# Kernel tuning notes

Measured on AMD Instinct MI355X. Metric: run time of the kernel, lower is better.

## Reference

```python
import jax, jax.numpy as jnp
import numpy as np

N_SRC0, N_DST0, N_DST1 = 100000, 50000, 25000
E0, E1, D = 1600000, 800000, 128


def setup_inputs() -> dict:
    key = jax.random.key(0)
    k = jax.random.split(key, 8)
    return {
        "x": jax.random.normal(k[0], (N_SRC0, D), dtype=jnp.float32),
        "src0": jax.random.randint(k[1], (E0,), 0, N_SRC0, dtype=jnp.int32),
        "dst0": jax.random.randint(k[2], (E0,), 0, N_DST0, dtype=jnp.int32),
        "ew0": jax.random.uniform(k[3], (E0,), dtype=jnp.float32),
        "src1": jax.random.randint(k[4], (E1,), 0, N_DST0, dtype=jnp.int32),
        "dst1": jax.random.randint(k[5], (E1,), 0, N_DST1, dtype=jnp.int32),
        "ew1": jax.random.uniform(k[6], (E1,), dtype=jnp.float32),
        "n_dst0": N_DST0,
        "n_dst1": N_DST1,
    }


def _propagate(h, src, dst, ew, n_dst):
    # u_mul_e: gather src feature per edge and scale by edge weight; sum-reduce to dst
    m = h[src] * ew[:, None]                      # [E, D]
    return jax.ops.segment_sum(m, dst, num_segments=n_dst)  # [n_dst, D]


def reference(x, src0, dst0, ew0, src1, dst1, ew1, n_dst0, n_dst1):
    # LightGCN forward over 2 sampled blocks, mlp_list=None
    h = _propagate(x, src0, dst0, ew0, n_dst0)    # [n_dst0, D]
    h = _propagate(h, src1, dst1, ew1, n_dst1)    # [n_dst1, D]
    return h
```

## Files before the change

### kernel.cpp

```cpp
#include <hip/hip_runtime.h>


#define DIMS 128
#define BK   64
#define BKSH 6
#define CAP  4096
#define CH   8192

__device__ __forceinline__ unsigned bf16_1(float a) {
  unsigned u = __float_as_uint(a);
  return (u + 0x7fffu + ((u >> 16) & 1u)) >> 16;
}
__device__ __forceinline__ unsigned pack_bf16(float a, float b) {
  return bf16_1(a) | (bf16_1(b) << 16);
}

__global__ __launch_bounds__(256) void hist_cvt(
    const int* __restrict__ dst0, const int* __restrict__ dst1,
    const float* __restrict__ xf, uint4* __restrict__ xbf4,
    int* __restrict__ wgcnt0, int* __restrict__ wgcnt1,
    int E0, int E1, int NB0, int NB1, int NW0, int NW1, long long n8) {
  int b = blockIdx.x;
  if (b < NW0 + NW1) {
    __shared__ int hist[1024];
    const int s1 = (b >= NW0);
    const int w  = s1 ? b - NW0 : b;
    const int E  = s1 ? E1 : E0;
    const int NB = s1 ? NB1 : NB0;
    const int* dst = s1 ? dst1 : dst0;
    int* wgcnt = s1 ? wgcnt1 : wgcnt0;
    for (int i = threadIdx.x; i < NB; i += 256) hist[i] = 0;
    __syncthreads();
    const int beg = w * CH, end = min(beg + CH, E);
    for (int e = beg + threadIdx.x; e < end; e += 256)
      atomicAdd(&hist[dst[e] >> BKSH], 1);
    __syncthreads();
    for (int i = threadIdx.x; i < NB; i += 256)
      wgcnt[w * NB + i] = hist[i];
  } else {
    long long t = (long long)(b - NW0 - NW1) * 256 + threadIdx.x;
    if (t < n8) {
      const float4* xf4 = (const float4*)xf;
      float4 v0 = xf4[t * 2], v1 = xf4[t * 2 + 1];
      xbf4[t] = make_uint4(pack_bf16(v0.x, v0.y), pack_bf16(v0.z, v0.w),
                           pack_bf16(v1.x, v1.y), pack_bf16(v1.z, v1.w));
    }
  }
}

__global__ __launch_bounds__(256) void scan_cols(
    int* __restrict__ wgcnt0, int* __restrict__ wgcnt1,
    int* __restrict__ gcur, int2* __restrict__ rg0, int2* __restrict__ rg1,
    int NB0, int NB1, int NW0, int NW1) {
  __shared__ int part[256];
  int b = blockIdx.x;
  const int s1 = (b >= NB0);
  const int i = s1 ? b - NB0 : b;
  int* wgcnt = s1 ? wgcnt1 : wgcnt0;
  int2* rg   = s1 ? rg1 : rg0;
  const int NB = s1 ? NB1 : NB0;
  const int NW = s1 ? NW1 : NW0;
  const int t = threadIdx.x;
  int v = (t < NW) ? wgcnt[t * NB + i] : 0;
  part[t] = v;
  __syncthreads();
  for (int off = 1; off < 256; off <<= 1) {
    int u = (t >= off) ? part[t - off] : 0;
    __syncthreads();
    part[t] += u;
    __syncthreads();
  }
  if (t < NW) wgcnt[t * NB + i] = part[t] - v;
  if (t == 255) {
    int tot = part[255];
    int base = atomicAdd(&gcur[s1], tot);
    rg[i] = make_int2(base, base + tot);
  }
}

__global__ __launch_bounds__(512) void partition_k(
    const int* __restrict__ src0, const int* __restrict__ dst0,
    const float* __restrict__ ew0, const int* __restrict__ src1,
    const int* __restrict__ dst1, const float* __restrict__ ew1,
    const int* __restrict__ wgcnt0, const int* __restrict__ wgcnt1,
    const int2* __restrict__ rg0, const int2* __restrict__ rg1,
    int2* __restrict__ payl0, int2* __restrict__ payl1,
    int E0, int E1, int NB0, int NB1, int NW0, int NW1) {
  __shared__ int cur[1024];
  int b = blockIdx.x;
  const int s1 = (b >= NW0);
  const int w  = s1 ? b - NW0 : b;
  const int E  = s1 ? E1 : E0;
  const int NB = s1 ? NB1 : NB0;
  const int* src = s1 ? src1 : src0;
  const int* dst = s1 ? dst1 : dst0;
  const float* ew = s1 ? ew1 : ew0;
  const int* wgcnt = s1 ? wgcnt1 : wgcnt0;
  const int2* rg = s1 ? rg1 : rg0;
  int2* payl = s1 ? payl1 : payl0;
  for (int i = threadIdx.x; i < NB; i += 512)
    cur[i] = rg[i].x + wgcnt[w * NB + i];
  __syncthreads();
  const int beg = w * CH, end = min(beg + CH, E);
  for (int e = beg + threadIdx.x; e < end; e += 512) {
    int d = dst[e];
    int pos = atomicAdd(&cur[d >> BKSH], 1);
    payl[pos] = make_int2(src[e],
                          (int)((bf16_1(ew[e]) << 16) | (unsigned)(d & (BK - 1))));
  }
}

#define EDGE_BLOCK(p, wgt, u)                                   \
  {                                                             \
    a0 += __uint_as_float((u).x << 16) * (wgt);                 \
    a1 += __uint_as_float((u).x & 0xffff0000u) * (wgt);         \
    a2 += __uint_as_float((u).y << 16) * (wgt);                 \
    a3 += __uint_as_float((u).y & 0xffff0000u) * (wgt);         \
    a4 += __uint_as_float((u).z << 16) * (wgt);                 \
    a5 += __uint_as_float((u).z & 0xffff0000u) * (wgt);         \
    a6 += __uint_as_float((u).w << 16) * (wgt);                 \
    a7 += __uint_as_float((u).w & 0xffff0000u) * (wgt);         \
  }

template <bool OUT_BF16>
__global__ __launch_bounds__(512) void gather_bkt(
    const uint4* __restrict__ feat, const int2* __restrict__ rg,
    const int2* __restrict__ payl, void* __restrict__ outp, int n_dst) {
  __shared__ int2 lp[CAP];
  __shared__ int cnt[BK], base[BK], cnt2[BK];
  const int b = blockIdx.x;
  const int tid = threadIdx.x;
  const int2 r = rg[b];
  const int n = r.y - r.x;
  const int nin = min(n, CAP);
  if (tid < BK) { cnt[tid] = 0; cnt2[tid] = 0; }
  __syncthreads();
  for (int j = tid; j < nin; j += 512)
    atomicAdd(&cnt[payl[r.x + j].y & (BK - 1)], 1);
  __syncthreads();
  if (tid < 64) {
    int v = cnt[tid];
    int s = v;
    for (int off = 1; off < 64; off <<= 1) {
      int u = __shfl_up(s, off);
      if (tid >= off) s += u;
    }
    base[tid] = s - v;
  }
  __syncthreads();
  for (int j = tid; j < nin; j += 512) {
    int2 p = payl[r.x + j];
    int dl = p.y & (BK - 1);
    int pos = base[dl] + atomicAdd(&cnt2[dl], 1);
    lp[pos] = p;
  }
  __syncthreads();
  const int wave = tid >> 6;
  const int lane = tid & 63;
  const int rr = lane >> 4;
  const int c  = lane & 15;
  for (int dl = wave; dl < BK; dl += 8) {
    const int row = b * BK + dl;
    if (row >= n_dst) break;
    const int bg = base[dl];
    const int en = bg + cnt[dl];
    float a0 = 0.f, a1 = 0.f, a2 = 0.f, a3 = 0.f;
    float a4 = 0.f, a5 = 0.f, a6 = 0.f, a7 = 0.f;
    for (int j = bg; j < en; j += 16) {
      const int jj0 = j + rr;
      const int jj1 = j + 4 + rr;
      const int jj2 = j + 8 + rr;
      const int jj3 = j + 12 + rr;
      int2 p0 = (jj0 < en) ? lp[jj0] : make_int2(0, 0);
      int2 p1 = (jj1 < en) ? lp[jj1] : make_int2(0, 0);
      int2 p2 = (jj2 < en) ? lp[jj2] : make_int2(0, 0);
      int2 p3 = (jj3 < en) ? lp[jj3] : make_int2(0, 0);
      uint4 u0 = feat[(size_t)p0.x * 16 + c];
      uint4 u1 = feat[(size_t)p1.x * 16 + c];
      uint4 u2 = feat[(size_t)p2.x * 16 + c];
      uint4 u3 = feat[(size_t)p3.x * 16 + c];
      float w0 = __uint_as_float((unsigned)p0.y & 0xffff0000u);
      float w1 = __uint_as_float((unsigned)p1.y & 0xffff0000u);
      float w2 = __uint_as_float((unsigned)p2.y & 0xffff0000u);
      float w3 = __uint_as_float((unsigned)p3.y & 0xffff0000u);
      EDGE_BLOCK(p0, w0, u0);
      EDGE_BLOCK(p1, w1, u1);
      EDGE_BLOCK(p2, w2, u2);
      EDGE_BLOCK(p3, w3, u3);
    }
    if (n > CAP) {
      for (int j = CAP; j < n; j += 4) {
        int jj = j + rr;
        int2 p = (jj < n) ? payl[r.x + jj] : make_int2(0, 0);
        bool mine = (jj < n) && ((p.y & (BK - 1)) == dl);
        float wgt = mine ? __uint_as_float((unsigned)p.y & 0xffff0000u) : 0.f;
        uint4 u = feat[(size_t)p.x * 16 + c];
        EDGE_BLOCK(p, wgt, u);
      }
    }
    a0 += __shfl_xor(a0, 16); a0 += __shfl_xor(a0, 32);
    a1 += __shfl_xor(a1, 16); a1 += __shfl_xor(a1, 32);
    a2 += __shfl_xor(a2, 16); a2 += __shfl_xor(a2, 32);
    a3 += __shfl_xor(a3, 16); a3 += __shfl_xor(a3, 32);
    a4 += __shfl_xor(a4, 16); a4 += __shfl_xor(a4, 32);
    a5 += __shfl_xor(a5, 16); a5 += __shfl_xor(a5, 32);
    a6 += __shfl_xor(a6, 16); a6 += __shfl_xor(a6, 32);
    a7 += __shfl_xor(a7, 16); a7 += __shfl_xor(a7, 32);
    if (OUT_BF16) {
      if (rr == 0) {
        ((uint4*)outp)[(size_t)row * 16 + c] =
            make_uint4(pack_bf16(a0, a1), pack_bf16(a2, a3),
                       pack_bf16(a4, a5), pack_bf16(a6, a7));
      }
    } else {
      if (rr < 2) {
        ((float4*)outp)[(size_t)row * 32 + c * 2 + rr] =
            (rr == 0) ? make_float4(a0, a1, a2, a3)
                      : make_float4(a4, a5, a6, a7);
      }
    }
  }
}

#define COLG 32
__global__ __launch_bounds__(256) void prop_atomic(
    const float* __restrict__ x, const int* __restrict__ src,
    const int* __restrict__ dst, const float* __restrict__ ew,
    float* __restrict__ out, int E) {
  long long idx = (long long)blockIdx.x * blockDim.x + threadIdx.x;
  long long total = (long long)E * COLG;
  if (idx >= total) return;
  int e = (int)(idx >> 5);
  int cg = (int)(idx & 31);
  int s = src[e];
  int d = dst[e];
  float w = ew[e];
  const float4 v = *reinterpret_cast<const float4*>(x + (size_t)s * DIMS + cg * 4);
  float* o = out + (size_t)d * DIMS + cg * 4;
  atomicAdd(o + 0, v.x * w);
  atomicAdd(o + 1, v.y * w);
  atomicAdd(o + 2, v.z * w);
  atomicAdd(o + 3, v.w * w);
}


static inline size_t align_up(size_t v, size_t a) { return (v + a - 1) / a * a; }

extern "C" void kernel_launch(void* const* d_in, const int* in_sizes, int n_in,
                              void* d_out, int out_size, void* d_ws, size_t ws_size,
                              hipStream_t stream) {
  const float* x    = (const float*)d_in[0];
  const int*   src0 = (const int*)d_in[1];
  const int*   dst0 = (const int*)d_in[2];
  const float* ew0  = (const float*)d_in[3];
  const int*   src1 = (const int*)d_in[4];
  const int*   dst1 = (const int*)d_in[5];
  const float* ew1  = (const float*)d_in[6];

  const int N_SRC0 = in_sizes[0] / DIMS;
  const int E0 = in_sizes[1];
  const int E1 = in_sizes[4];
  const int N_DST0 = 50000;
  const int N_DST1 = 25000;

  const int NB0 = (N_DST0 + BK - 1) / BK;
  const int NB1 = (N_DST1 + BK - 1) / BK;
  const int NW0 = (E0 + CH - 1) / CH;
  const int NW1 = (E1 + CH - 1) / CH;

  float* out = (float*)d_out;

  char* ws = (char*)d_ws;
  size_t off = 0;
  uint4* xb    = (uint4*)(ws + off); off = align_up(off + (size_t)N_SRC0 * 64 * 4, 16);
  uint4* hb    = (uint4*)(ws + off); off = align_up(off + (size_t)N_DST0 * 64 * 4, 16);
  int* wgcnt0  = (int*)(ws + off);   off = align_up(off + (size_t)NW0 * NB0 * 4, 16);
  int* wgcnt1  = (int*)(ws + off);   off = align_up(off + (size_t)NW1 * NB1 * 4, 16);
  int* gcur    = (int*)(ws + off);   off = align_up(off + 2 * 4, 16);
  int2* rg0    = (int2*)(ws + off);  off = align_up(off + (size_t)NB0 * 8, 16);
  int2* rg1    = (int2*)(ws + off);  off = align_up(off + (size_t)NB1 * 8, 16);
  int2* payl0  = (int2*)(ws + off);  off = align_up(off + (size_t)E0 * 8, 16);
  int2* payl1  = (int2*)(ws + off);  off = align_up(off + (size_t)E1 * 8, 16);
  const size_t needed = off;

  if (ws_size < needed) {
    float* h = (float*)d_ws;
    hipMemsetAsync(h, 0, (size_t)N_DST0 * DIMS * 4, stream);
    hipMemsetAsync(out, 0, (size_t)N_DST1 * DIMS * 4, stream);
    long long t0 = (long long)E0 * COLG;
    prop_atomic<<<(int)((t0 + 255) / 256), 256, 0, stream>>>(x, src0, dst0, ew0, h, E0);
    long long t1 = (long long)E1 * COLG;
    prop_atomic<<<(int)((t1 + 255) / 256), 256, 0, stream>>>(h, src1, dst1, ew1, out, E1);
    return;
  }

  const long long n8 = (long long)N_SRC0 * 16;
  const int cvtBlocks = (int)((n8 + 255) / 256);

  hipMemsetAsync(gcur, 0, 2 * 4, stream);

  hist_cvt<<<NW0 + NW1 + cvtBlocks, 256, 0, stream>>>(
      dst0, dst1, x, xb, wgcnt0, wgcnt1, E0, E1, NB0, NB1, NW0, NW1, n8);

  scan_cols<<<NB0 + NB1, 256, 0, stream>>>(wgcnt0, wgcnt1, gcur, rg0, rg1,
                                           NB0, NB1, NW0, NW1);

  partition_k<<<NW0 + NW1, 512, 0, stream>>>(
      src0, dst0, ew0, src1, dst1, ew1, wgcnt0, wgcnt1, rg0, rg1,
      payl0, payl1, E0, E1, NB0, NB1, NW0, NW1);

  gather_bkt<true><<<NB0, 512, 0, stream>>>(xb, rg0, payl0, (void*)hb, N_DST0);

  gather_bkt<false><<<NB1, 512, 0, stream>>>(hb, rg1, payl1, (void*)out, N_DST1);
}
```

Baseline: 168.9 us.

## Quantize gathered node features to int8 with per-row scales

Replaces the bf16 copies of the input features and the intermediate layer with int8 values plus a per-row float scale. The row scale is folded into the edge weight when payloads are staged in shared memory. This halves the bytes fetched per gathered row in both random-access gather passes, at the cost of much lower precision, which may break accuracy tolerances. It also swizzles the chunk-to-block mapping in the histogram and partition kernels, and the main gather loop loses its 4-way unroll.

Result: no change. 169.3 us (+0.2%).

```diff
diff --git a/kernel.cpp b/kernel.cpp
--- a/kernel.cpp
+++ b/kernel.cpp
@@ -11,20 +11,23 @@
   unsigned u = __float_as_uint(a);
   return (u + 0x7fffu + ((u >> 16) & 1u)) >> 16;
 }
-__device__ __forceinline__ unsigned pack_bf16(float a, float b) {
-  return bf16_1(a) | (bf16_1(b) << 16);
+
+__device__ __forceinline__ int chunk_swz(int b, int NW) {
+  const int q = NW >> 3, r = NW & 7, x = b & 7;
+  return (x < r ? x * (q + 1) : r * (q + 1) + (x - r) * q) + (b >> 3);
 }
 
 __global__ __launch_bounds__(256) void hist_cvt(
     const int* __restrict__ dst0, const int* __restrict__ dst1,
-    const float* __restrict__ xf, uint4* __restrict__ xbf4,
+    const float* __restrict__ xf, uint2* __restrict__ xq,
+    float* __restrict__ xscale,
     int* __restrict__ wgcnt0, int* __restrict__ wgcnt1,
-    int E0, int E1, int NB0, int NB1, int NW0, int NW1, long long n8) {
+    int E0, int E1, int NB0, int NB1, int NW0, int NW1, int NSRC) {
   int b = blockIdx.x;
   if (b < NW0 + NW1) {
     __shared__ int hist[1024];
     const int s1 = (b >= NW0);
-    const int w  = s1 ? b - NW0 : b;
+    const int w  = s1 ? chunk_swz(b - NW0, NW1) : chunk_swz(b, NW0);
     const int E  = s1 ? E1 : E0;
     const int NB = s1 ? NB1 : NB0;
     const int* dst = s1 ? dst1 : dst0;
@@ -38,12 +41,31 @@
     for (int i = threadIdx.x; i < NB; i += 256)
       wgcnt[w * NB + i] = hist[i];
   } else {
-    long long t = (long long)(b - NW0 - NW1) * 256 + threadIdx.x;
-    if (t < n8) {
+    int gi = (b - NW0 - NW1) * 256 + threadIdx.x;
+    int row = gi >> 4, c = gi & 15;
+    if (row < NSRC) {
       const float4* xf4 = (const float4*)xf;
-      float4 v0 = xf4[t * 2], v1 = xf4[t * 2 + 1];
-      xbf4[t] = make_uint4(pack_bf16(v0.x, v0.y), pack_bf16(v0.z, v0.w),
-                           pack_bf16(v1.x, v1.y), pack_bf16(v1.z, v1.w));
+      float4 v0 = xf4[(size_t)row * 32 + c * 2];
+      float4 v1 = xf4[(size_t)row * 32 + c * 2 + 1];
+      float m = fmaxf(fmaxf(fmaxf(fabsf(v0.x), fabsf(v0.y)),
+                            fmaxf(fabsf(v0.z), fabsf(v0.w))),
+                      fmaxf(fmaxf(fabsf(v1.x), fabsf(v1.y)),
+                            fmaxf(fabsf(v1.z), fabsf(v1.w))));
+      m = fmaxf(m, __shfl_xor(m, 1));
+      m = fmaxf(m, __shfl_xor(m, 2));
+      m = fmaxf(m, __shfl_xor(m, 4));
+      m = fmaxf(m, __shfl_xor(m, 8));
+      float inv = (m > 0.f) ? 127.0f / m : 0.f;
+      int q0 = (int)rintf(v0.x * inv), q1 = (int)rintf(v0.y * inv);
+      int q2 = (int)rintf(v0.z * inv), q3 = (int)rintf(v0.w * inv);
+      int q4 = (int)rintf(v1.x * inv), q5 = (int)rintf(v1.y * inv);
+      int q6 = (int)rintf(v1.z * inv), q7 = (int)rintf(v1.w * inv);
+      unsigned lo = (q0 & 255) | ((q1 & 255) << 8) |
+                    ((q2 & 255) << 16) | ((q3 & 255) << 24);
+      unsigned hi = (q4 & 255) | ((q5 & 255) << 8) |
+                    ((q6 & 255) << 16) | ((q7 & 255) << 24);
+      xq[(size_t)row * 16 + c] = make_uint2(lo, hi);
+      if (c == 0) xscale[row] = m * (1.0f / 127.0f);
     }
   }
 }
@@ -89,7 +111,7 @@
   __shared__ int cur[1024];
   int b = blockIdx.x;
   const int s1 = (b >= NW0);
-  const int w  = s1 ? b - NW0 : b;
+  const int w  = s1 ? chunk_swz(b - NW0, NW1) : chunk_swz(b, NW0);
   const int E  = s1 ? E1 : E0;
   const int NB = s1 ? NB1 : NB0;
   const int* src = s1 ? src1 : src0;
@@ -110,22 +132,23 @@
   }
 }
 
-#define EDGE_BLOCK(p, wgt, u)                                   \
+#define EDGE_BLOCK8(ws, u)                                      \
   {                                                             \
-    a0 += __uint_as_float((u).x << 16) * (wgt);                 \
-    a1 += __uint_as_float((u).x & 0xffff0000u) * (wgt);         \
-    a2 += __uint_as_float((u).y << 16) * (wgt);                 \
-    a3 += __uint_as_float((u).y & 0xffff0000u) * (wgt);         \
-    a4 += __uint_as_float((u).z << 16) * (wgt);                 \
-    a5 += __uint_as_float((u).z & 0xffff0000u) * (wgt);         \
-    a6 += __uint_as_float((u).w << 16) * (wgt);                 \
-    a7 += __uint_as_float((u).w & 0xffff0000u) * (wgt);         \
-  }
-
-template <bool OUT_BF16>
+    a0 += (float)((int)((u).x << 24) >> 24) * (ws);             \
+    a1 += (float)((int)((u).x << 16) >> 24) * (ws);             \
+    a2 += (float)((int)((u).x << 8) >> 24) * (ws);              \
+    a3 += (float)((int)(u).x >> 24) * (ws);                     \
+    a4 += (float)((int)((u).y << 24) >> 24) * (ws);             \
+    a5 += (float)((int)((u).y << 16) >> 24) * (ws);             \
+    a6 += (float)((int)((u).y << 8) >> 24) * (ws);              \
+    a7 += (float)((int)(u).y >> 24) * (ws);                     \
+  }
+
+template <bool OUT_I8>
 __global__ __launch_bounds__(512) void gather_bkt(
-    const uint4* __restrict__ feat, const int2* __restrict__ rg,
-    const int2* __restrict__ payl, void* __restrict__ outp, int n_dst) {
+    const uint2* __restrict__ feat, const float* __restrict__ scl,
+    const int2* __restrict__ rg, const int2* __restrict__ payl,
+    void* __restrict__ outp, float* __restrict__ oscale, int n_dst) {
   __shared__ int2 lp[CAP];
   __shared__ int cnt[BK], base[BK], cnt2[BK];
   const int b = blockIdx.x;
@@ -151,8 +174,9 @@
   for (int j = tid; j < nin; j += 512) {
     int2 p = payl[r.x + j];
     int dl = p.y & (BK - 1);
+    float ws = __uint_as_float((unsigned)p.y & 0xffff0000u) * scl[p.x];
     int pos = base[dl] + atomicAdd(&cnt2[dl], 1);
-    lp[pos] = p;
+    lp[pos] = make_int2(p.x, (int)((bf16_1(ws) << 16) | (unsigned)dl));
   }
   __syncthreads();
   const int wave = tid >> 6;
@@ -166,36 +190,22 @@
     const int en = bg + cnt[dl];
     float a0 = 0.f, a1 = 0.f, a2 = 0.f, a3 = 0.f;
     float a4 = 0.f, a5 = 0.f, a6 = 0.f, a7 = 0.f;
-    for (int j = bg; j < en; j += 16) {
-      const int jj0 = j + rr;
-      const int jj1 = j + 4 + rr;
-      const int jj2 = j + 8 + rr;
-      const int jj3 = j + 12 + rr;
-      int2 p0 = (jj0 < en) ? lp[jj0] : make_int2(0, 0);
-      int2 p1 = (jj1 < en) ? lp[jj1] : make_int2(0, 0);
-      int2 p2 = (jj2 < en) ? lp[jj2] : make_int2(0, 0);
-      int2 p3 = (jj3 < en) ? lp[jj3] : make_int2(0, 0);
-      uint4 u0 = feat[(size_t)p0.x * 16 + c];
-      uint4 u1 = feat[(size_t)p1.x * 16 + c];
-      uint4 u2 = feat[(size_t)p2.x * 16 + c];
-      uint4 u3 = feat[(size_t)p3.x * 16 + c];
-      float w0 = __uint_as_float((unsigned)p0.y & 0xffff0000u);
-      float w1 = __uint_as_float((unsigned)p1.y & 0xffff0000u);
-      float w2 = __uint_as_float((unsigned)p2.y & 0xffff0000u);
-      float w3 = __uint_as_float((unsigned)p3.y & 0xffff0000u);
-      EDGE_BLOCK(p0, w0, u0);
-      EDGE_BLOCK(p1, w1, u1);
-      EDGE_BLOCK(p2, w2, u2);
-      EDGE_BLOCK(p3, w3, u3);
+    for (int j = bg; j < en; j += 4) {
+      int jj = j + rr;
+      int2 p = (jj < en) ? lp[jj] : make_int2(0, 0);
+      float ws = __uint_as_float((unsigned)p.y & 0xffff0000u);
+      uint2 u = feat[(size_t)p.x * 16 + c];
+      EDGE_BLOCK8(ws, u);
     }
     if (n > CAP) {
       for (int j = CAP; j < n; j += 4) {
         int jj = j + rr;
         int2 p = (jj < n) ? payl[r.x + jj] : make_int2(0, 0);
         bool mine = (jj < n) && ((p.y & (BK - 1)) == dl);
-        float wgt = mine ? __uint_as_float((unsigned)p.y & 0xffff0000u) : 0.f;
-        uint4 u = feat[(size_t)p.x * 16 + c];
-        EDGE_BLOCK(p, wgt, u);
+        float ws = mine
+            ? __uint_as_float((unsigned)p.y & 0xffff0000u) * scl[p.x] : 0.f;
+        uint2 u = feat[(size_t)p.x * 16 + c];
+        EDGE_BLOCK8(ws, u);
       }
     }
     a0 += __shfl_xor(a0, 16); a0 += __shfl_xor(a0, 32);
@@ -206,12 +216,30 @@
     a5 += __shfl_xor(a5, 16); a5 += __shfl_xor(a5, 32);
     a6 += __shfl_xor(a6, 16); a6 += __shfl_xor(a6, 32);
     a7 += __shfl_xor(a7, 16); a7 += __shfl_xor(a7, 32);
-    if (OUT_BF16) {
+    if (OUT_I8) {
+      float m = fmaxf(fmaxf(fmaxf(fabsf(a0), fabsf(a1)),
+                            fmaxf(fabsf(a2), fabsf(a3))),
+                      fmaxf(fmaxf(fabsf(a4), fabsf(a5)),
+                            fmaxf(fabsf(a6), fabsf(a7))));
+      m = fmaxf(m, __shfl_xor(m, 1));
+      m = fmaxf(m, __shfl_xor(m, 2));
+      m = fmaxf(m, __shfl_xor(m, 4));
+      m = fmaxf(m, __shfl_xor(m, 8));
+      m = fmaxf(m, __shfl_xor(m, 16));
+      m = fmaxf(m, __shfl_xor(m, 32));
+      float inv = (m > 0.f) ? 127.0f / m : 0.f;
       if (rr == 0) {
-        ((uint4*)outp)[(size_t)row * 16 + c] =
-            make_uint4(pack_bf16(a0, a1), pack_bf16(a2, a3),
-                       pack_bf16(a4, a5), pack_bf16(a6, a7));
+        int q0 = (int)rintf(a0 * inv), q1 = (int)rintf(a1 * inv);
+        int q2 = (int)rintf(a2 * inv), q3 = (int)rintf(a3 * inv);
+        int q4 = (int)rintf(a4 * inv), q5 = (int)rintf(a5 * inv);
+        int q6 = (int)rintf(a6 * inv), q7 = (int)rintf(a7 * inv);
+        unsigned lo = (q0 & 255) | ((q1 & 255) << 8) |
+                      ((q2 & 255) << 16) | ((q3 & 255) << 24);
+        unsigned hi = (q4 & 255) | ((q5 & 255) << 8) |
+                      ((q6 & 255) << 16) | ((q7 & 255) << 24);
+        ((uint2*)outp)[(size_t)row * 16 + c] = make_uint2(lo, hi);
       }
+      if (lane == 0) oscale[row] = m * (1.0f / 127.0f);
     } else {
       if (rr < 2) {
         ((float4*)outp)[(size_t)row * 32 + c * 2 + rr] =
@@ -272,15 +300,17 @@
 
   char* ws = (char*)d_ws;
   size_t off = 0;
-  uint4* xb    = (uint4*)(ws + off); off = align_up(off + (size_t)N_SRC0 * 64 * 4, 16);
-  uint4* hb    = (uint4*)(ws + off); off = align_up(off + (size_t)N_DST0 * 64 * 4, 16);
-  int* wgcnt0  = (int*)(ws + off);   off = align_up(off + (size_t)NW0 * NB0 * 4, 16);
-  int* wgcnt1  = (int*)(ws + off);   off = align_up(off + (size_t)NW1 * NB1 * 4, 16);
-  int* gcur    = (int*)(ws + off);   off = align_up(off + 2 * 4, 16);
-  int2* rg0    = (int2*)(ws + off);  off = align_up(off + (size_t)NB0 * 8, 16);
-  int2* rg1    = (int2*)(ws + off);  off = align_up(off + (size_t)NB1 * 8, 16);
-  int2* payl0  = (int2*)(ws + off);  off = align_up(off + (size_t)E0 * 8, 16);
-  int2* payl1  = (int2*)(ws + off);  off = align_up(off + (size_t)E1 * 8, 16);
+  uint2* xq     = (uint2*)(ws + off); off = align_up(off + (size_t)N_SRC0 * 16 * 8, 16);
+  float* xscale = (float*)(ws + off); off = align_up(off + (size_t)N_SRC0 * 4, 16);
+  uint2* hq     = (uint2*)(ws + off); off = align_up(off + (size_t)N_DST0 * 16 * 8, 16);
+  float* hscale = (float*)(ws + off); off = align_up(off + (size_t)N_DST0 * 4, 16);
+  int* wgcnt0   = (int*)(ws + off);   off = align_up(off + (size_t)NW0 * NB0 * 4, 16);
+  int* wgcnt1   = (int*)(ws + off);   off = align_up(off + (size_t)NW1 * NB1 * 4, 16);
+  int* gcur     = (int*)(ws + off);   off = align_up(off + 2 * 4, 16);
+  int2* rg0     = (int2*)(ws + off);  off = align_up(off + (size_t)NB0 * 8, 16);
+  int2* rg1     = (int2*)(ws + off);  off = align_up(off + (size_t)NB1 * 8, 16);
+  int2* payl0   = (int2*)(ws + off);  off = align_up(off + (size_t)E0 * 8, 16);
+  int2* payl1   = (int2*)(ws + off);  off = align_up(off + (size_t)E1 * 8, 16);
   const size_t needed = off;
 
   if (ws_size < needed) {
@@ -294,13 +324,13 @@
     return;
   }
 
-  const long long n8 = (long long)N_SRC0 * 16;
-  const int cvtBlocks = (int)((n8 + 255) / 256);
+  const int cvtBlocks = (N_SRC0 * 16 + 255) / 256;
 
   hipMemsetAsync(gcur, 0, 2 * 4, stream);
 
   hist_cvt<<<NW0 + NW1 + cvtBlocks, 256, 0, stream>>>(
-      dst0, dst1, x, xb, wgcnt0, wgcnt1, E0, E1, NB0, NB1, NW0, NW1, n8);
+      dst0, dst1, x, xq, xscale, wgcnt0, wgcnt1,
+      E0, E1, NB0, NB1, NW0, NW1, N_SRC0);
 
   scan_cols<<<NB0 + NB1, 256, 0, stream>>>(wgcnt0, wgcnt1, gcur, rg0, rg1,
                                            NB0, NB1, NW0, NW1);
@@ -309,7 +339,9 @@
       src0, dst0, ew0, src1, dst1, ew1, wgcnt0, wgcnt1, rg0, rg1,
       payl0, payl1, E0, E1, NB0, NB1, NW0, NW1);
 
-  gather_bkt<true><<<NB0, 512, 0, stream>>>(xb, rg0, payl0, (void*)hb, N_DST0);
-
-  gather_bkt<false><<<NB1, 512, 0, stream>>>(hb, rg1, payl1, (void*)out, N_DST1);
-}
+  gather_bkt<true><<<NB0, 512, 0, stream>>>(
+      xq, xscale, rg0, payl0, (void*)hq, hscale, N_DST0);
+
+  gather_bkt<false><<<NB1, 512, 0, stream>>>(
+      hq, hscale, rg1, payl1, (void*)out, (float*)nullptr, N_DST1);
+}
```

## Process two destination rows per wave in gather and swizzle chunk order

Applied to the files above, without the earlier changes.

Each wave in the bucketed gather kernel now accumulates two destination rows at once (dl and dl+8), interleaving their edge loads. This gives two independent gather streams per iteration instead of a four-way unroll over one row's edge list, which cuts tail waste for short rows and balances per-row degree. It also permutes which edge chunk each workgroup handles in the histogram and partition kernels so that consecutive blocks touch spread-out chunks. The cost is more accumulator registers and more lanes idle when the two rows differ in degree.

Measured after the change: 168.5 us. About the same (-0.3%).

```diff
diff --git a/kernel.cpp b/kernel.cpp
--- a/kernel.cpp
+++ b/kernel.cpp
@@ -13,6 +13,11 @@
 }
 __device__ __forceinline__ unsigned pack_bf16(float a, float b) {
   return bf16_1(a) | (bf16_1(b) << 16);
+}
+
+__device__ __forceinline__ int chunk_swz(int b, int NW) {
+  const int q = NW >> 3, r = NW & 7, x = b & 7;
+  return (x < r ? x * (q + 1) : r * (q + 1) + (x - r) * q) + (b >> 3);
 }
 
 __global__ __launch_bounds__(256) void hist_cvt(
@@ -24,7 +29,7 @@
   if (b < NW0 + NW1) {
     __shared__ int hist[1024];
     const int s1 = (b >= NW0);
-    const int w  = s1 ? b - NW0 : b;
+    const int w  = s1 ? chunk_swz(b - NW0, NW1) : chunk_swz(b, NW0);
     const int E  = s1 ? E1 : E0;
     const int NB = s1 ? NB1 : NB0;
     const int* dst = s1 ? dst1 : dst0;
@@ -89,7 +94,7 @@
   __shared__ int cur[1024];
   int b = blockIdx.x;
   const int s1 = (b >= NW0);
-  const int w  = s1 ? b - NW0 : b;
+  const int w  = s1 ? chunk_swz(b - NW0, NW1) : chunk_swz(b, NW0);
   const int E  = s1 ? E1 : E0;
   const int NB = s1 ? NB1 : NB0;
   const int* src = s1 ? src1 : src0;
@@ -110,7 +115,7 @@
   }
 }
 
-#define EDGE_BLOCK(p, wgt, u)                                   \
+#define ACC8(a0,a1,a2,a3,a4,a5,a6,a7, wgt, u)                   \
   {                                                             \
     a0 += __uint_as_float((u).x << 16) * (wgt);                 \
     a1 += __uint_as_float((u).x & 0xffff0000u) * (wgt);         \
@@ -159,43 +164,41 @@
   const int lane = tid & 63;
   const int rr = lane >> 4;
   const int c  = lane & 15;
-  for (int dl = wave; dl < BK; dl += 8) {
-    const int row = b * BK + dl;
-    if (row >= n_dst) break;
-    const int bg = base[dl];
-    const int en = bg + cnt[dl];
+  for (int dl = wave; dl < BK; dl += 16) {
+    const int rowA = b * BK + dl;
+    const int rowB = b * BK + dl + 8;
+    if (rowA >= n_dst) break;
+    const bool hasB = (rowB < n_dst);
+    const int bgA = base[dl];
+    const int lA = cnt[dl];
+    const int bgB = hasB ? base[dl + 8] : 0;
+    const int lB = hasB ? cnt[dl + 8] : 0;
+    const int lmax = max(lA, lB);
     float a0 = 0.f, a1 = 0.f, a2 = 0.f, a3 = 0.f;
     float a4 = 0.f, a5 = 0.f, a6 = 0.f, a7 = 0.f;
-    for (int j = bg; j < en; j += 16) {
-      const int jj0 = j + rr;
-      const int jj1 = j + 4 + rr;
-      const int jj2 = j + 8 + rr;
-      const int jj3 = j + 12 + rr;
-      int2 p0 = (jj0 < en) ? lp[jj0] : make_int2(0, 0);
-      int2 p1 = (jj1 < en) ? lp[jj1] : make_int2(0, 0);
-      int2 p2 = (jj2 < en) ? lp[jj2] : make_int2(0, 0);
-      int2 p3 = (jj3 < en) ? lp[jj3] : make_int2(0, 0);
-      uint4 u0 = feat[(size_t)p0.x * 16 + c];
-      uint4 u1 = feat[(size_t)p1.x * 16 + c];
-      uint4 u2 = feat[(size_t)p2.x * 16 + c];
-      uint4 u3 = feat[(size_t)p3.x * 16 + c];
-      float w0 = __uint_as_float((unsigned)p0.y & 0xffff0000u);
-      float w1 = __uint_as_float((unsigned)p1.y & 0xffff0000u);
-      float w2 = __uint_as_float((unsigned)p2.y & 0xffff0000u);
-      float w3 = __uint_as_float((unsigned)p3.y & 0xffff0000u);
-      EDGE_BLOCK(p0, w0, u0);
-      EDGE_BLOCK(p1, w1, u1);
-      EDGE_BLOCK(p2, w2, u2);
-      EDGE_BLOCK(p3, w3, u3);
+    float b0 = 0.f, b1 = 0.f, b2 = 0.f, b3 = 0.f;
+    float b4 = 0.f, b5 = 0.f, b6 = 0.f, b7 = 0.f;
+    for (int k = rr; k < lmax; k += 4) {
+      int2 pA = (k < lA) ? lp[bgA + k] : make_int2(0, 0);
+      int2 pB = (k < lB) ? lp[bgB + k] : make_int2(0, 0);
+      uint4 uA = feat[(size_t)pA.x * 16 + c];
+      uint4 uB = feat[(size_t)pB.x * 16 + c];
+      float wA = __uint_as_float((unsigned)pA.y & 0xffff0000u);
+      float wB = __uint_as_float((unsigned)pB.y & 0xffff0000u);
+      ACC8(a0, a1, a2, a3, a4, a5, a6, a7, wA, uA);
+      ACC8(b0, b1, b2, b3, b4, b5, b6, b7, wB, uB);
     }
     if (n > CAP) {
-      for (int j = CAP; j < n; j += 4) {
-        int jj = j + rr;
-        int2 p = (jj < n) ? payl[r.x + jj] : make_int2(0, 0);
-        bool mine = (jj < n) && ((p.y & (BK - 1)) == dl);
-        float wgt = mine ? __uint_as_float((unsigned)p.y & 0xffff0000u) : 0.f;
+      for (int j = CAP + rr; j < n; j += 4) {
+        int2 p = payl[r.x + j];
+        int pdl = p.y & (BK - 1);
+        float wA = (pdl == dl)
+            ? __uint_as_float((unsigned)p.y & 0xffff0000u) : 0.f;
+        float wB = (hasB && pdl == dl + 8)
+            ? __uint_as_float((unsigned)p.y & 0xffff0000u) : 0.f;
         uint4 u = feat[(size_t)p.x * 16 + c];
-        EDGE_BLOCK(p, wgt, u);
+        ACC8(a0, a1, a2, a3, a4, a5, a6, a7, wA, u);
+        ACC8(b0, b1, b2, b3, b4, b5, b6, b7, wB, u);
       }
     }
     a0 += __shfl_xor(a0, 16); a0 += __shfl_xor(a0, 32);
@@ -206,17 +209,33 @@
     a5 += __shfl_xor(a5, 16); a5 += __shfl_xor(a5, 32);
     a6 += __shfl_xor(a6, 16); a6 += __shfl_xor(a6, 32);
     a7 += __shfl_xor(a7, 16); a7 += __shfl_xor(a7, 32);
+    b0 += __shfl_xor(b0, 16); b0 += __shfl_xor(b0, 32);
+    b1 += __shfl_xor(b1, 16); b1 += __shfl_xor(b1, 32);
+    b2 += __shfl_xor(b2, 16); b2 += __shfl_xor(b2, 32);
+    b3 += __shfl_xor(b3, 16); b3 += __shfl_xor(b3, 32);
+    b4 += __shfl_xor(b4, 16); b4 += __shfl_xor(b4, 32);
+    b5 += __shfl_xor(b5, 16); b5 += __shfl_xor(b5, 32);
+    b6 += __shfl_xor(b6, 16); b6 += __shfl_xor(b6, 32);
+    b7 += __shfl_xor(b7, 16); b7 += __shfl_xor(b7, 32);
     if (OUT_BF16) {
       if (rr == 0) {
-        ((uint4*)outp)[(size_t)row * 16 + c] =
+        ((uint4*)outp)[(size_t)rowA * 16 + c] =
             make_uint4(pack_bf16(a0, a1), pack_bf16(a2, a3),
                        pack_bf16(a4, a5), pack_bf16(a6, a7));
+        if (hasB)
+          ((uint4*)outp)[(size_t)rowB * 16 + c] =
+              make_uint4(pack_bf16(b0, b1), pack_bf16(b2, b3),
+                         pack_bf16(b4, b5), pack_bf16(b6, b7));
       }
     } else {
       if (rr < 2) {
-        ((float4*)outp)[(size_t)row * 32 + c * 2 + rr] =
+        ((float4*)outp)[(size_t)rowA * 32 + c * 2 + rr] =
             (rr == 0) ? make_float4(a0, a1, a2, a3)
                       : make_float4(a4, a5, a6, a7);
+        if (hasB)
+          ((float4*)outp)[(size_t)rowB * 32 + c * 2 + rr] =
+              (rr == 0) ? make_float4(b0, b1, b2, b3)
+                        : make_float4(b4, b5, b6, b7);
       }
     }
   }
```
